# Kernel optimization log

Measured on AMD Instinct MI355X. Metric: run time of the kernel, lower is better.

Reference implementation:

```python
import jax, jax.numpy as jnp
import numpy as np

B, S, H, V = 2, 2048, 1024, 32000
SDS = [64, 128, 256]
EPS = 1e-5


def _ln(x, g, b):
    m = jnp.mean(x, -1, keepdims=True)
    v = jnp.var(x, -1, keepdims=True)
    return (x - m) * jax.lax.rsqrt(v + EPS) * g + b


def _layer(x, A_log, Wb, Wc, D, Wg, bg, Wo, bo, g, be):
    # x: [B,S,H]; state dim N = A_log.shape[0]
    A = jnp.exp(A_log)
    gate = jax.nn.sigmoid(jnp.einsum('bsh,nh->bsn', x, Wg) + bg)
    Bx = jnp.einsum('bsh,nh->bsn', x, Wb)
    u = gate * Bx  # [B,S,N]

    def step(s, u_t):
        s = A * s + u_t
        return s, s

    s0 = jnp.zeros((x.shape[0], A.shape[0]), x.dtype)
    _, states = jax.lax.scan(step, s0, jnp.swapaxes(u, 0, 1))  # [S,B,N]
    states = jnp.swapaxes(states, 0, 1)
    y = jnp.einsum('bsn,hn->bsh', states, Wc) + D * x
    out = _ln(y + x, g, be)
    return out @ Wo.T + bo  # dropout is identity (p used in eval / p=0)


def setup_inputs() -> dict:
    key = jax.random.key(0)
    ks = iter(jax.random.split(key, 64))
    d = {}
    d['x'] = jax.random.randint(next(ks), (B, S), 0, V)
    d['E'] = jax.random.normal(next(ks), (V, H), jnp.float32) * 0.02
    for i, N in enumerate(SDS):
        d[f'A{i}'] = jnp.log(jnp.exp(jnp.full((N,), -0.5)) + 0.1 * jax.random.normal(next(ks), (N,)))
        d[f'Wb{i}'] = jax.random.normal(next(ks), (N, H), jnp.float32) * 0.02
        d[f'Wc{i}'] = jax.random.normal(next(ks), (H, N), jnp.float32) * 0.02
        d[f'D{i}'] = jax.random.normal(next(ks), (H,), jnp.float32)
        d[f'Wg{i}'] = jax.random.normal(next(ks), (N, H), jnp.float32) * 0.02
        d[f'bg{i}'] = jnp.zeros((N,), jnp.float32)
        d[f'Wo{i}'] = jax.random.normal(next(ks), (H, H), jnp.float32) * 0.02
        d[f'bo{i}'] = jnp.zeros((H,), jnp.float32)
        d[f'g{i}'] = jnp.ones((H,), jnp.float32)
        d[f'be{i}'] = jnp.zeros((H,), jnp.float32)
    d['Wf'] = jax.random.normal(next(ks), (H, 3 * H), jnp.float32) * 0.02
    d['bf'] = jnp.zeros((H,), jnp.float32)
    d['gf'] = jnp.ones((H,), jnp.float32)
    d['bef'] = jnp.zeros((H,), jnp.float32)
    d['Wh'] = jax.random.normal(next(ks), (V, H), jnp.float32) * 0.02
    d['bh'] = jnp.zeros((V,), jnp.float32)
    return d


def reference(x, E,
              A0, Wb0, Wc0, D0, Wg0, bg0, Wo0, bo0, g0, be0,
              A1, Wb1, Wc1, D1, Wg1, bg1, Wo1, bo1, g1, be1,
              A2, Wb2, Wc2, D2, Wg2, bg2, Wo2, bo2, g2, be2,
              Wf, bf, gf, bef, Wh, bh):
    emb = E[x]  # [B,S,H]
    o0 = _layer(emb, A0, Wb0, Wc0, D0, Wg0, bg0, Wo0, bo0, g0, be0)
    o1 = _layer(emb, A1, Wb1, Wc1, D1, Wg1, bg1, Wo1, bo1, g1, be1)
    o2 = _layer(emb, A2, Wb2, Wc2, D2, Wg2, bg2, Wo2, bo2, g2, be2)
    combined = jnp.concatenate([o0, o1, o2], axis=-1)  # [B,S,3H]
    fused = combined @ Wf.T + bf
    fused = _ln(fused + emb, gf, bef)
    logits = fused @ Wh.T + bh  # [B,S,V]
    return logits
```

## Files before the change

### kernel.cpp

```cpp
#include <hip/hip_runtime.h>
#include <hip/hip_bf16.h>

#define Hd 1024
#define Bdim 2
#define Sd 2048
#define BSd 4096
#define Vd 32000
#define EPSf 1e-5f
#define CH 16
#define NCH 128
#define NT3 448

typedef __attribute__((ext_vector_type(8))) short short8;
typedef __attribute__((ext_vector_type(4))) float f32x4;
typedef __attribute__((ext_vector_type(4))) unsigned short us4;

__device__ __forceinline__ unsigned short f2bf(float f) {
  union { float f; unsigned int u; } v; v.f = f;
  return (unsigned short)((v.u + 0x7fffu + ((v.u >> 16) & 1u)) >> 16);
}

typedef __attribute__((address_space(1))) const void gvoid_t;
typedef __attribute__((address_space(3))) void svoid_t;
__device__ __forceinline__ void gl_lds16(const void* g, void* s) {
  __builtin_amdgcn_global_load_lds((gvoid_t*)g, (svoid_t*)s, 16, 0, 0);
}

struct CvtTab {
  const float* src[11];
  unsigned short* dst[11];
  int start[12];
};
__global__ void k_cvt_all(CvtTab tab) {
  int b = blockIdx.x;
  int j = 0;
  while (j < 10 && b >= tab.start[j + 1]) ++j;
  size_t i = (size_t)(b - tab.start[j]) * 256 + threadIdx.x;
  f32x4 v = *(const f32x4*)(tab.src[j] + i * 4);
  us4 o;
  o[0] = f2bf(v[0]); o[1] = f2bf(v[1]); o[2] = f2bf(v[2]); o[3] = f2bf(v[3]);
  *(us4*)(tab.dst[j] + i * 4) = o;
}

__global__ void k_cvtT(const float* __restrict__ s0, const float* __restrict__ s1,
                       const float* __restrict__ s2, unsigned short* __restrict__ dst) {
  const float* src = blockIdx.z == 0 ? s0 : (blockIdx.z == 1 ? s1 : s2);
  unsigned short* d = dst + (size_t)blockIdx.z * Hd * Hd;
  __shared__ float tile[32][33];
  int tx = threadIdx.x & 31, ty = threadIdx.x >> 5;
  int bx = blockIdx.x * 32, by = blockIdx.y * 32;
  #pragma unroll
  for (int i = 0; i < 4; ++i)
    tile[ty + i * 8][tx] = src[(size_t)(by + ty + i * 8) * Hd + bx + tx];
  __syncthreads();
  #pragma unroll
  for (int i = 0; i < 4; ++i)
    d[(size_t)(bx + ty + i * 8) * Hd + by + tx] = f2bf(tile[tx][ty + i * 8]);
}

__global__ void k_biasf(const float* __restrict__ Wf_, const float* __restrict__ bfb,
                        const float* __restrict__ bo0, const float* __restrict__ bo1,
                        const float* __restrict__ bo2, float* __restrict__ biasf) {
  int h = blockIdx.x, t = threadIdx.x;
  float s = 0.f;
  for (int c = t; c < 3072; c += 256) {
    float b = c < 1024 ? bo0[c] : (c < 2048 ? bo1[c - 1024] : bo2[c - 2048]);
    s += Wf_[(size_t)h * 3072 + c] * b;
  }
  #pragma unroll
  for (int o = 32; o >= 1; o >>= 1) s += __shfl_xor(s, o);
  __shared__ float red[4];
  if ((t & 63) == 0) red[t >> 6] = s;
  __syncthreads();
  if (t == 0) biasf[h] = bfb[h] + red[0] + red[1] + red[2] + red[3];
}

__global__ void k_setup(const float* A0, const float* A1, const float* A2,
                        const float* b0, const float* b1, const float* b2,
                        const float* D0, const float* D1, const float* D2,
                        const float* g0, const float* g1, const float* g2,
                        const float* e0, const float* e1, const float* e2,
                        float* Alog448, float* bg448,
                        float* D3, float* g3, float* be3) {
  int t = blockIdx.x * 256 + threadIdx.x;
  if (t < NT3) {
    int l = t < 64 ? 0 : (t < 192 ? 1 : 2);
    int o = t - (l == 0 ? 0 : (l == 1 ? 64 : 192));
    Alog448[t] = (l == 0 ? A0 : (l == 1 ? A1 : A2))[o];
    bg448[t]   = (l == 0 ? b0 : (l == 1 ? b1 : b2))[o];
  }
  if (t < 3072) {
    int l = t >> 10, o = t & 1023;
    D3[t]  = (l == 0 ? D0 : (l == 1 ? D1 : D2))[o];
    g3[t]  = (l == 0 ? g0 : (l == 1 ? g1 : g2))[o];
    be3[t] = (l == 0 ? e0 : (l == 1 ? e1 : e2))[o];
  }
}

__global__ void k_embed(const int* __restrict__ x, const float* __restrict__ E,
                        float* __restrict__ emb, unsigned short* __restrict__ embbf) {
  int row = blockIdx.x, t = threadIdx.x;
  int id = x[row];
  f32x4 v = *(const f32x4*)(E + (size_t)id * Hd + t * 4);
  *(f32x4*)(emb + (size_t)row * Hd + t * 4) = v;
  us4 o;
  o[0] = f2bf(v[0]); o[1] = f2bf(v[1]); o[2] = f2bf(v[2]); o[3] = f2bf(v[3]);
  *(us4*)(embbf + (size_t)row * Hd + t * 4) = o;
}

template<int BM, int BN, int WM, int WN, int BF16_OUT>
__launch_bounds__(WM * WN * 64)
__global__ void gemm2ph(const unsigned short* __restrict__ A,
                        const unsigned short* __restrict__ Bw,
                        const float* __restrict__ bias,
                        void* __restrict__ Cv,
                        int N, int K, int lda, int ldb, int ldc, int coff, int tm)
{
  constexpr int NT = WM * WN * 64;
  constexpr int MF = BM / WM / 16;
  constexpr int NF = BN / WN / 16;
  constexpr int ASZ = BM * 64;
  constexpr int BSZ = BN * 64;
  constexpr int AR = (ASZ * 2) / (NT * 16);
  constexpr int BR = (BSZ * 2) / (NT * 16);
  __shared__ __align__(16) unsigned short Sm[2 * (ASZ + BSZ)];

  int T = gridDim.x;
  int orig = blockIdx.x;
  int q = T >> 3, r = T & 7;
  int xc = orig & 7, sdv = orig >> 3;
  int wgid = (xc < r ? xc * (q + 1) : r * (q + 1) + (xc - r) * q) + sdv;
  int n_t = wgid / tm, m_t = wgid % tm;
  int row0 = m_t * BM, col0 = n_t * BN;

  int tid = threadIdx.x;
  int wave = tid >> 6, lane = tid & 63;
  int wm = wave / WN, wn = wave % WN;
  int wr = wm * (BM / WM), wc = wn * (BN / WN);
  int lr = lane & 15;
  int klane = lane >> 4;

  f32x4 acc[MF][NF] = {};

  auto stage = [&](int buf, int k0) {
    unsigned short* Ab = Sm + buf * (ASZ + BSZ);
    unsigned short* Bb = Ab + ASZ;
    #pragma unroll
    for (int j = 0; j < AR; ++j) {
      int slot = j * NT + tid;
      int lrow = slot >> 3, c16 = slot & 7;
      int scol = (c16 ^ (lrow & 7)) * 8;
      gl_lds16(A + (size_t)(row0 + lrow) * lda + k0 + scol, Ab + (j * NT + wave * 64) * 8);
    }
    #pragma unroll
    for (int j = 0; j < BR; ++j) {
      int slot = j * NT + tid;
      int lrow = slot >> 3, c16 = slot & 7;
      int scol = (c16 ^ (lrow & 7)) * 8;
      int brow = col0 + lrow;
      if (brow >= N) brow = N - 1;
      gl_lds16(Bw + (size_t)brow * ldb + k0 + scol, Bb + (j * NT + wave * 64) * 8);
    }
  };

  auto compute = [&](int buf) {
    const unsigned short* Ab = Sm + buf * (ASZ + BSZ);
    const unsigned short* Bb = Ab + ASZ;
    #pragma unroll
    for (int kk = 0; kk < 2; ++kk) {
      short8 afr[MF], bfr[NF];
      #pragma unroll
      for (int m = 0; m < MF; ++m) {
        int row = wr + m * 16 + lr;
        int cs = (kk * 4 + klane) ^ (row & 7);
        afr[m] = *(const short8*)(Ab + row * 64 + cs * 8);
      }
      #pragma unroll
      for (int n = 0; n < NF; ++n) {
        int row = wc + n * 16 + lr;
        int cs = (kk * 4 + klane) ^ (row & 7);
        bfr[n] = *(const short8*)(Bb + row * 64 + cs * 8);
      }
      #pragma unroll
      for (int m = 0; m < MF; ++m)
        #pragma unroll
        for (int n = 0; n < NF; ++n)
          acc[m][n] = __builtin_amdgcn_mfma_f32_16x16x32_bf16(afr[m], bfr[n], acc[m][n], 0, 0, 0);
    }
  };

  int nt = K >> 6;
  stage(0, 0);
  __syncthreads();
  for (int t = 0; t < nt - 1; ++t) {
    stage((t & 1) ^ 1, (t + 1) * 64);
    compute(t & 1);
    __syncthreads();
  }
  compute((nt - 1) & 1);

  int rb = (lane >> 4) * 4;
  #pragma unroll
  for (int m = 0; m < MF; ++m) {
    #pragma unroll
    for (int n = 0; n < NF; ++n) {
      int gcol = col0 + wc + n * 16 + lr;
      if (gcol >= N) continue;
      float bv = bias ? bias[gcol] : 0.f;
      #pragma unroll
      for (int j = 0; j < 4; ++j) {
        int grow = row0 + wr + m * 16 + rb + j;
        float val = acc[m][n][j] + bv;
        if (BF16_OUT)
          ((unsigned short*)Cv)[(size_t)grow * ldc + coff + gcol] = f2bf(val);
        else
          ((float*)Cv)[(size_t)grow * ldc + coff + gcol] = val;
      }
    }
  }
}

__launch_bounds__(512)
__global__ void gemm_ring(const unsigned short* __restrict__ A,
                          const unsigned short* __restrict__ Bw,
                          const float* __restrict__ bias,
                          float* __restrict__ Cv,
                          int N, int K, int lda, int ldb, int ldc, int tm)
{
  constexpr int ASZ = 256 * 32;
  constexpr int BUF = 2 * ASZ;
  __shared__ __align__(16) unsigned short Sm[4 * BUF];

  int T = gridDim.x;
  int orig = blockIdx.x;
  int q = T >> 3, r = T & 7;
  int xc = orig & 7, sdv = orig >> 3;
  int wgid = (xc < r ? xc * (q + 1) : r * (q + 1) + (xc - r) * q) + sdv;
  int n_t = wgid / tm, m_t = wgid % tm;
  int row0 = m_t * 256, col0 = n_t * 256;

  int tid = threadIdx.x;
  int wave = tid >> 6, lane = tid & 63;
  int wm = wave >> 2, wn = wave & 3;
  int wr = wm * 128, wc = wn * 64;
  int lr = lane & 15, klane = lane >> 4;

  f32x4 acc[8][4] = {};

  auto stage = [&](int buf, int kt) {
    int k0 = kt * 32;
    unsigned short* Ab = Sm + buf * BUF;
    unsigned short* Bb = Ab + ASZ;
    #pragma unroll
    for (int j = 0; j < 2; ++j) {
      int slot = j * 512 + wave * 64 + lane;
      int rrow = slot >> 2, ck = (slot & 3) * 8;
      gl_lds16(A + (size_t)(row0 + rrow) * lda + k0 + ck, Ab + (j * 512 + wave * 64) * 8);
    }
    #pragma unroll
    for (int j = 0; j < 2; ++j) {
      int slot = j * 512 + wave * 64 + lane;
      int rrow = slot >> 2, ck = (slot & 3) * 8;
      int brow = col0 + rrow;
      if (brow >= N) brow = N - 1;
      gl_lds16(Bw + (size_t)brow * ldb + k0 + ck, Bb + (j * 512 + wave * 64) * 8);
    }
  };

  auto compute = [&](int buf) {
    const unsigned short* Ab = Sm + buf * BUF;
    const unsigned short* Bb = Ab + ASZ;
    short8 afr[8], bfr[4];
    #pragma unroll
    for (int m = 0; m < 8; ++m)
      afr[m] = *(const short8*)(Ab + (wr + m * 16 + lr) * 32 + klane * 8);
    #pragma unroll
    for (int n = 0; n < 4; ++n)
      bfr[n] = *(const short8*)(Bb + (wc + n * 16 + lr) * 32 + klane * 8);
    __builtin_amdgcn_s_setprio(1);
    #pragma unroll
    for (int m = 0; m < 8; ++m)
      #pragma unroll
      for (int n = 0; n < 4; ++n)
        acc[m][n] = __builtin_amdgcn_mfma_f32_16x16x32_bf16(afr[m], bfr[n], acc[m][n], 0, 0, 0);
    __builtin_amdgcn_s_setprio(0);
  };

  int nt = K >> 5;
  stage(0, 0); stage(1, 1); stage(2, 2);
  for (int t = 0; t < nt; ++t) {
    if (t < nt - 2)       asm volatile("s_waitcnt vmcnt(8)" ::: "memory");
    else if (t == nt - 2) asm volatile("s_waitcnt vmcnt(4)" ::: "memory");
    else                  asm volatile("s_waitcnt vmcnt(0)" ::: "memory");
    __builtin_amdgcn_s_barrier();
    if (t + 3 < nt) stage((t + 3) & 3, t + 3);
    compute(t & 3);
  }

  int rb = (lane >> 4) * 4;
  #pragma unroll
  for (int m = 0; m < 8; ++m) {
    #pragma unroll
    for (int n = 0; n < 4; ++n) {
      int gcol = col0 + wc + n * 16 + lr;
      if (gcol >= N) continue;
      float bv = bias ? bias[gcol] : 0.f;
      #pragma unroll
      for (int j = 0; j < 4; ++j) {
        int grow = row0 + wr + m * 16 + rb + j;
        Cv[(size_t)grow * ldc + gcol] = acc[m][n][j] + bv;
      }
    }
  }
}

__global__ void k_scanA(const float* __restrict__ gzbx, const float* __restrict__ Alog448,
                        const float* __restrict__ bg448,
                        float* __restrict__ st, float* __restrict__ carry) {
  int gid = blockIdx.x * 256 + threadIdx.x;
  if (gid >= Bdim * NCH * NT3) return;
  int n = gid % NT3;
  int c = (gid / NT3) % NCH;
  int b = gid / (NT3 * NCH);
  float a = expf(Alog448[n]);
  float bgv = bg448[n];
  float s = 0.f;
  size_t rbase = (size_t)b * Sd + (size_t)c * CH;
  for (int t = 0; t < CH; ++t) {
    size_t row = rbase + t;
    float gzv = gzbx[row * 896 + n];
    float bxv = gzbx[row * 896 + 448 + n];
    float gv = 1.f / (1.f + expf(-(gzv + bgv)));
    s = a * s + gv * bxv;
    st[row * NT3 + n] = s;
  }
  carry[((size_t)b * NCH + c) * NT3 + n] = s;
}

__global__ void k_scanB(const float* __restrict__ carry, const float* __restrict__ Alog448,
                        float* __restrict__ cin) {
  int i = blockIdx.x * 256 + threadIdx.x;
  if (i >= Bdim * NT3) return;
  int b = i / NT3, n = i % NT3;
  float aC = expf((float)CH * Alog448[n]);
  float s = 0.f;
  for (int c = 0; c < NCH; ++c) {
    cin[((size_t)b * NCH + c) * NT3 + n] = s;
    s = aC * s + carry[((size_t)b * NCH + c) * NT3 + n];
  }
}

__global__ void k_scanC(const float* __restrict__ st, const float* __restrict__ cin,
                        const float* __restrict__ Alog448, unsigned short* __restrict__ stbf) {
  size_t gid = (size_t)blockIdx.x * 256 + threadIdx.x;
  if (gid >= (size_t)BSd * NT3) return;
  int n = gid % NT3;
  int row = gid / NT3;
  int b = row / Sd, sg = row % Sd;
  int c = sg / CH, t = sg % CH;
  float cv = cin[((size_t)b * NCH + c) * NT3 + n];
  float val = st[gid] + expf((float)(t + 1) * Alog448[n]) * cv;
  stbf[gid] = f2bf(val);
}

__global__ void k_ln3(const float* __restrict__ y3, const float* __restrict__ emb,
                      const float* __restrict__ D3, const float* __restrict__ g3,
                      const float* __restrict__ be3, unsigned short* __restrict__ z3) {
  int row = blockIdx.x, ly = blockIdx.y, t = threadIdx.x;
  const float* y = y3 + (size_t)row * 3072 + ly * 1024;
  f32x4 yv = *(const f32x4*)(y + t * 4);
  f32x4 ev = *(const f32x4*)(emb + (size_t)row * Hd + t * 4);
  float vals[4];
  float sum = 0.f, sq = 0.f;
  #pragma unroll
  for (int j = 0; j < 4; ++j) {
    float coef = D3[ly * 1024 + t * 4 + j] + 1.f;
    float v = yv[j] + coef * ev[j];
    vals[j] = v; sum += v; sq += v * v;
  }
  #pragma unroll
  for (int o = 32; o >= 1; o >>= 1) {
    sum += __shfl_xor(sum, o);
    sq += __shfl_xor(sq, o);
  }
  __shared__ float red[2][4];
  int w = t >> 6, lane = t & 63;
  if (lane == 0) { red[0][w] = sum; red[1][w] = sq; }
  __syncthreads();
  sum = red[0][0] + red[0][1] + red[0][2] + red[0][3];
  sq  = red[1][0] + red[1][1] + red[1][2] + red[1][3];
  float mean = sum * (1.f / Hd);
  float var = sq * (1.f / Hd) - mean * mean;
  float rs = rsqrtf(var + EPSf);
  us4 o4;
  #pragma unroll
  for (int j = 0; j < 4; ++j) {
    float z = (vals[j] - mean) * rs * g3[ly * 1024 + t * 4 + j] + be3[ly * 1024 + t * 4 + j];
    o4[j] = f2bf(z);
  }
  *(us4*)(z3 + (size_t)row * 3072 + ly * 1024 + t * 4) = o4;
}

__global__ void k_ln(const float* __restrict__ y, const float* __restrict__ emb,
                     const float* __restrict__ g, const float* __restrict__ be,
                     unsigned short* __restrict__ out) {
  int row = blockIdx.x, t = threadIdx.x;
  f32x4 yv = *(const f32x4*)(y + (size_t)row * Hd + t * 4);
  f32x4 ev = *(const f32x4*)(emb + (size_t)row * Hd + t * 4);
  float vals[4];
  float sum = 0.f, sq = 0.f;
  #pragma unroll
  for (int j = 0; j < 4; ++j) {
    float v = yv[j] + ev[j];
    vals[j] = v; sum += v; sq += v * v;
  }
  #pragma unroll
  for (int o = 32; o >= 1; o >>= 1) {
    sum += __shfl_xor(sum, o);
    sq += __shfl_xor(sq, o);
  }
  __shared__ float red[2][4];
  int w = t >> 6, lane = t & 63;
  if (lane == 0) { red[0][w] = sum; red[1][w] = sq; }
  __syncthreads();
  sum = red[0][0] + red[0][1] + red[0][2] + red[0][3];
  sq  = red[1][0] + red[1][1] + red[1][2] + red[1][3];
  float mean = sum * (1.f / Hd);
  float var = sq * (1.f / Hd) - mean * mean;
  float rs = rsqrtf(var + EPSf);
  us4 o4;
  #pragma unroll
  for (int j = 0; j < 4; ++j) {
    float z = (vals[j] - mean) * rs * g[t * 4 + j] + be[t * 4 + j];
    o4[j] = f2bf(z);
  }
  *(us4*)(out + (size_t)row * Hd + t * 4) = o4;
}

extern "C" void kernel_launch(void* const* d_in, const int* in_sizes, int n_in,
                              void* d_out, int out_size, void* d_ws, size_t ws_size,
                              hipStream_t stream) {
  (void)in_sizes; (void)n_in; (void)out_size; (void)ws_size;
  const int* x = (const int*)d_in[0];
  const float* E = (const float*)d_in[1];
  const float* Wf_ = (const float*)d_in[32];
  const float* bfb = (const float*)d_in[33];
  const float* gfp = (const float*)d_in[34];
  const float* bef = (const float*)d_in[35];
  const float* Wh_ = (const float*)d_in[36];
  const float* bh = (const float*)d_in[37];

  char* wsb = (char*)d_ws;
  size_t off = 0;
  auto alloc = [&](size_t bytes) -> void* {
    void* p = wsb + off;
    off += (bytes + 255) & ~(size_t)255;
    return p;
  };
  float* emb             = (float*)alloc((size_t)BSd * Hd * 4);
  unsigned short* embbf  = (unsigned short*)alloc((size_t)BSd * Hd * 2);
  unsigned short* wgwbbf = (unsigned short*)alloc((size_t)896 * Hd * 2);
  unsigned short* wcbf   = (unsigned short*)alloc((size_t)NT3 * Hd * 2);
  unsigned short* wotbf  = (unsigned short*)alloc((size_t)3 * Hd * Hd * 2);
  unsigned short* wfbf   = (unsigned short*)alloc((size_t)3 * Hd * Hd * 2);
  unsigned short* wcombbf= (unsigned short*)alloc((size_t)Hd * 3 * Hd * 2);
  unsigned short* whbf   = (unsigned short*)alloc((size_t)Vd * Hd * 2);
  float* gzbx            = (float*)alloc((size_t)BSd * 896 * 4);
  float* stl             = (float*)alloc((size_t)BSd * NT3 * 4);
  unsigned short* stbf   = (unsigned short*)alloc((size_t)BSd * NT3 * 2);
  float* carry           = (float*)alloc((size_t)Bdim * NCH * NT3 * 4);
  float* cin             = (float*)alloc((size_t)Bdim * NCH * NT3 * 4);
  float* ybuf3           = (float*)alloc((size_t)BSd * 3072 * 4);
  unsigned short* zbf3   = (unsigned short*)alloc((size_t)BSd * 3072 * 2);
  unsigned short* zbf    = (unsigned short*)alloc((size_t)BSd * Hd * 2);
  float* Alog448         = (float*)alloc(NT3 * 4);
  float* bg448           = (float*)alloc(NT3 * 4);
  float* D3              = (float*)alloc(3072 * 4);
  float* g3              = (float*)alloc(3072 * 4);
  float* be3             = (float*)alloc(3072 * 4);
  float* biasf           = (float*)alloc(Hd * 4);

  k_embed<<<BSd, 256, 0, stream>>>(x, E, emb, embbf);

  {
    CvtTab tab;
    const int rowoff_g[3] = {0, 64, 192};
    int j = 0;
    int n4s[11];
    for (int i = 0; i < 3; ++i) { tab.src[j] = (const float*)d_in[2 + 10 * i + 4]; tab.dst[j] = wgwbbf + (size_t)rowoff_g[i] * Hd;         n4s[j] = (64 << i) * Hd / 4; ++j; }
    for (int i = 0; i < 3; ++i) { tab.src[j] = (const float*)d_in[2 + 10 * i + 1]; tab.dst[j] = wgwbbf + (size_t)(448 + rowoff_g[i]) * Hd;  n4s[j] = (64 << i) * Hd / 4; ++j; }
    for (int i = 0; i < 3; ++i) { tab.src[j] = (const float*)d_in[2 + 10 * i + 2]; tab.dst[j] = wcbf + (size_t)rowoff_g[i] * Hd;            n4s[j] = (64 << i) * Hd / 4; ++j; }
    tab.src[j] = Wf_; tab.dst[j] = wfbf; n4s[j] = 3 * Hd * Hd / 4; ++j;
    tab.src[j] = Wh_; tab.dst[j] = whbf; n4s[j] = Vd * Hd / 4; ++j;
    tab.start[0] = 0;
    for (int k = 0; k < 11; ++k) tab.start[k + 1] = tab.start[k] + (n4s[k] + 255) / 256;
    k_cvt_all<<<tab.start[11], 256, 0, stream>>>(tab);
  }

  k_cvtT<<<dim3(32, 32, 3), 256, 0, stream>>>(
      (const float*)d_in[8], (const float*)d_in[18], (const float*)d_in[28], wotbf);

  k_setup<<<12, 256, 0, stream>>>(
      (const float*)d_in[2], (const float*)d_in[12], (const float*)d_in[22],
      (const float*)d_in[7], (const float*)d_in[17], (const float*)d_in[27],
      (const float*)d_in[5], (const float*)d_in[15], (const float*)d_in[25],
      (const float*)d_in[10], (const float*)d_in[20], (const float*)d_in[30],
      (const float*)d_in[11], (const float*)d_in[21], (const float*)d_in[31],
      Alog448, bg448, D3, g3, be3);

  k_biasf<<<Hd, 256, 0, stream>>>(Wf_, bfb,
      (const float*)d_in[9], (const float*)d_in[19], (const float*)d_in[29], biasf);

  for (int i = 0; i < 3; ++i) {
    gemm2ph<128,128,2,2,1><<<(Hd / 128) * (Hd / 128), 256, 0, stream>>>(
        wfbf + i * Hd, wotbf + (size_t)i * Hd * Hd, nullptr, wcombbf,
        Hd, Hd, 3 * Hd, Hd, 3 * Hd, i * Hd, Hd / 128);
  }

  const int TM = BSd / 128;

  gemm2ph<128,128,2,2,0><<<(896 / 128) * TM, 256, 0, stream>>>(
      embbf, wgwbbf, nullptr, gzbx, 896, Hd, Hd, Hd, 896, 0, TM);

  {
    int totA = Bdim * NCH * NT3;
    k_scanA<<<(totA + 255) / 256, 256, 0, stream>>>(gzbx, Alog448, bg448, stl, carry);
    k_scanB<<<(Bdim * NT3 + 255) / 256, 256, 0, stream>>>(carry, Alog448, cin);
    size_t totC = (size_t)BSd * NT3;
    k_scanC<<<(int)((totC + 255) / 256), 256, 0, stream>>>(stl, cin, Alog448, stbf);
  }

  const int owg[3] = {0, 64, 192};
  const int sd[3] = {64, 128, 256};
  for (int i = 0; i < 3; ++i) {
    gemm2ph<128,128,2,2,0><<<(Hd / 128) * TM, 256, 0, stream>>>(
        stbf + owg[i], wcbf + (size_t)owg[i] * Hd, nullptr, ybuf3,
        Hd, sd[i], NT3, sd[i], 3072, i * Hd, TM);
  }

  k_ln3<<<dim3(BSd, 3), 256, 0, stream>>>(ybuf3, emb, D3, g3, be3, zbf3);

  gemm2ph<128,128,2,2,0><<<(Hd / 128) * TM, 256, 0, stream>>>(
      zbf3, wcombbf, biasf, ybuf3, Hd, 3 * Hd, 3 * Hd, 3 * Hd, Hd, 0, TM);
  k_ln<<<BSd, 256, 0, stream>>>(ybuf3, emb, gfp, bef, zbf);

  const int TM256 = BSd / 256;
  gemm_ring<<<(Vd / 256) * TM256, 512, 0, stream>>>(
      zbf, whbf, bh, (float*)d_out, Vd, Hd, Hd, Hd, Vd, TM256);
}
```

Baseline: 648.7 us.

## Replace vocab-head GEMM with 8-phase ping-pong schedule and swizzled LDS

The final logits GEMM (4096x32000x1024) now uses K-tiles of 64 instead of 32, split into half-tiles, with an XOR-swizzled LDS layout meant to avoid bank conflicts. Each iteration runs eight barrier-separated phases that interleave LDS fragment reads, MFMA bursts and staged global-to-LDS loads across two buffers. The aim is finer overlap of memory traffic with MFMA work and fewer LDS conflicts on the dominant kernel. It drops the N-boundary clamping; 32000 divides by 256 so this holds here. It also adds many barriers and uses 128 KB of LDS.

```diff
diff --git a/kernel.cpp b/kernel.cpp
--- a/kernel.cpp
+++ b/kernel.cpp
@@ -221,15 +221,13 @@
 }
 
 __launch_bounds__(512)
-__global__ void gemm_ring(const unsigned short* __restrict__ A,
-                          const unsigned short* __restrict__ Bw,
-                          const float* __restrict__ bias,
-                          float* __restrict__ Cv,
-                          int N, int K, int lda, int ldb, int ldc, int tm)
+__global__ void gemm8ph(const unsigned short* __restrict__ A,
+                        const unsigned short* __restrict__ Bw,
+                        const float* __restrict__ bias,
+                        float* __restrict__ Cv,
+                        int N, int K, int lda, int ldb, int ldc, int tm)
 {
-  constexpr int ASZ = 256 * 32;
-  constexpr int BUF = 2 * ASZ;
-  __shared__ __align__(16) unsigned short Sm[4 * BUF];
+  __shared__ __align__(16) unsigned short Sm[65536];
 
   int T = gridDim.x;
   int orig = blockIdx.x;
@@ -242,76 +240,138 @@
   int tid = threadIdx.x;
   int wave = tid >> 6, lane = tid & 63;
   int wm = wave >> 2, wn = wave & 3;
-  int wr = wm * 128, wc = wn * 64;
   int lr = lane & 15, klane = lane >> 4;
 
   f32x4 acc[8][4] = {};
 
-  auto stage = [&](int buf, int kt) {
-    int k0 = kt * 32;
-    unsigned short* Ab = Sm + buf * BUF;
-    unsigned short* Bb = Ab + ASZ;
+  auto stageA = [&](int b, int h, int kt) {
+    unsigned short* base = Sm + (b * 2 + h) * 8192;
     #pragma unroll
     for (int j = 0; j < 2; ++j) {
-      int slot = j * 512 + wave * 64 + lane;
-      int rrow = slot >> 2, ck = (slot & 3) * 8;
-      gl_lds16(A + (size_t)(row0 + rrow) * lda + k0 + ck, Ab + (j * 512 + wave * 64) * 8);
-    }
+      int slot = j * 512 + tid;
+      int lrow = slot >> 3, c16 = slot & 7;
+      int scol = (c16 ^ (lrow & 7)) * 8;
+      gl_lds16(A + (size_t)(row0 + h * 128 + lrow) * lda + kt * 64 + scol,
+               base + (j * 512 + wave * 64) * 8);
+    }
+  };
+  auto stageB = [&](int b, int h, int kt) {
+    unsigned short* base = Sm + 32768 + (b * 2 + h) * 8192;
     #pragma unroll
     for (int j = 0; j < 2; ++j) {
-      int slot = j * 512 + wave * 64 + lane;
-      int rrow = slot >> 2, ck = (slot & 3) * 8;
-      int brow = col0 + rrow;
-      if (brow >= N) brow = N - 1;
-      gl_lds16(Bw + (size_t)brow * ldb + k0 + ck, Bb + (j * 512 + wave * 64) * 8);
+      int slot = j * 512 + tid;
+      int lrow = slot >> 3, c16 = slot & 7;
+      int scol = (c16 ^ (lrow & 7)) * 8;
+      gl_lds16(Bw + (size_t)(col0 + h * 128 + lrow) * ldb + kt * 64 + scol,
+               base + (j * 512 + wave * 64) * 8);
     }
   };
-
-  auto compute = [&](int buf) {
-    const unsigned short* Ab = Sm + buf * BUF;
-    const unsigned short* Bb = Ab + ASZ;
-    short8 afr[8], bfr[4];
-    #pragma unroll
-    for (int m = 0; m < 8; ++m)
-      afr[m] = *(const short8*)(Ab + (wr + m * 16 + lr) * 32 + klane * 8);
-    #pragma unroll
-    for (int n = 0; n < 4; ++n)
-      bfr[n] = *(const short8*)(Bb + (wc + n * 16 + lr) * 32 + klane * 8);
-    __builtin_amdgcn_s_setprio(1);
-    #pragma unroll
-    for (int m = 0; m < 8; ++m)
+  auto readA = [&](short8* afr, int b, int mh, int kk) {
+    const unsigned short* base = Sm + (b * 2 + mh) * 8192;
+    #pragma unroll
+    for (int f = 0; f < 4; ++f) {
+      int rowin = f * 32 + wm * 16 + lr;
+      int cs = (kk * 4 + klane) ^ (rowin & 7);
+      afr[f] = *(const short8*)(base + rowin * 64 + cs * 8);
+    }
+  };
+  auto readB = [&](short8* bfr, int b, int kk) {
+    #pragma unroll
+    for (int n = 0; n < 4; ++n) {
+      int rowin = (n & 1) * 64 + wn * 16 + lr;
+      const unsigned short* base = Sm + 32768 + (b * 2 + (n >> 1)) * 8192;
+      int cs = (kk * 4 + klane) ^ (rowin & 7);
+      bfr[n] = *(const short8*)(base + rowin * 64 + cs * 8);
+    }
+  };
+
+  #define MFMA16(mh, afr, bfr)                                                  \
+    __builtin_amdgcn_s_setprio(1);                                              \
+    _Pragma("unroll")                                                           \
+    for (int f = 0; f < 4; ++f)                                                 \
+      _Pragma("unroll")                                                         \
+      for (int n = 0; n < 4; ++n)                                               \
+        acc[(mh) * 4 + f][n] = __builtin_amdgcn_mfma_f32_16x16x32_bf16(         \
+            afr[f], bfr[n], acc[(mh) * 4 + f][n], 0, 0, 0);                     \
+    __builtin_amdgcn_s_setprio(0);
+
+  #define BAR()   __builtin_amdgcn_s_barrier()
+  #define FEN()   asm volatile("" ::: "memory")
+  #define VM4()   asm volatile("s_waitcnt vmcnt(4)" ::: "memory")
+  #define VM0()   asm volatile("s_waitcnt vmcnt(0)" ::: "memory")
+
+  int nt = K >> 6;
+  int iters = K >> 7;
+
+  stageA(0, 0, 0); stageB(0, 0, 0); stageB(0, 1, 0); stageA(0, 1, 0);
+  stageA(1, 0, 1); stageB(1, 0, 1);
+  VM4(); BAR();
+
+  short8 afr[4], bfr0[4], bfr1[4];
+  for (int i = 0; i < iters; ++i) {
+    int t1 = 2 * i + 1, t2 = 2 * i + 2, t3 = 2 * i + 3;
+    bool last = (i == iters - 1);
+    readA(afr, 0, 0, 0); readB(bfr0, 0, 0);
+    BAR(); FEN();
+    stageB(1, 1, t1); stageA(1, 1, t1);
+    MFMA16(0, afr, bfr0);
+    BAR();
+    readA(afr, 0, 0, 1); readB(bfr1, 0, 1);
+    BAR(); FEN();
+    MFMA16(0, afr, bfr1);
+    BAR();
+    readA(afr, 0, 1, 0);
+    BAR(); FEN();
+    if (t2 < nt) stageA(0, 0, t2);
+    MFMA16(1, afr, bfr0);
+    BAR();
+    readA(afr, 0, 1, 1);
+    BAR(); FEN();
+    if (t2 < nt) stageB(0, 0, t2);
+    MFMA16(1, afr, bfr1);
+    if (last) { VM0(); } else { VM4(); }
+    BAR();
+    readA(afr, 1, 0, 0); readB(bfr0, 1, 0);
+    BAR(); FEN();
+    if (t2 < nt) { stageB(0, 1, t2); stageA(0, 1, t2); }
+    MFMA16(0, afr, bfr0);
+    BAR();
+    readA(afr, 1, 0, 1); readB(bfr1, 1, 1);
+    BAR(); FEN();
+    MFMA16(0, afr, bfr1);
+    BAR();
+    readA(afr, 1, 1, 0);
+    BAR(); FEN();
+    if (t3 < nt) stageA(1, 0, t3);
+    MFMA16(1, afr, bfr0);
+    BAR();
+    readA(afr, 1, 1, 1);
+    BAR(); FEN();
+    if (t3 < nt) stageB(1, 0, t3);
+    MFMA16(1, afr, bfr1);
+    if (!last) { VM4(); }
+    BAR();
+  }
+
+  int rb = (lane >> 4) * 4;
+  #pragma unroll
+  for (int idx = 0; idx < 8; ++idx) {
+    int mh = idx >> 2, f = idx & 3;
+    int growb = row0 + mh * 128 + f * 32 + wm * 16 + rb;
+    #pragma unroll
+    for (int n = 0; n < 4; ++n) {
+      int gcol = col0 + (n & 1) * 64 + (n >> 1) * 128 + wn * 16 + lr;
+      float bv = bias[gcol];
       #pragma unroll
-      for (int n = 0; n < 4; ++n)
-        acc[m][n] = __builtin_amdgcn_mfma_f32_16x16x32_bf16(afr[m], bfr[n], acc[m][n], 0, 0, 0);
-    __builtin_amdgcn_s_setprio(0);
-  };
-
-  int nt = K >> 5;
-  stage(0, 0); stage(1, 1); stage(2, 2);
-  for (int t = 0; t < nt; ++t) {
-    if (t < nt - 2)       asm volatile("s_waitcnt vmcnt(8)" ::: "memory");
-    else if (t == nt - 2) asm volatile("s_waitcnt vmcnt(4)" ::: "memory");
-    else                  asm volatile("s_waitcnt vmcnt(0)" ::: "memory");
-    __builtin_amdgcn_s_barrier();
-    if (t + 3 < nt) stage((t + 3) & 3, t + 3);
-    compute(t & 3);
-  }
-
-  int rb = (lane >> 4) * 4;
-  #pragma unroll
-  for (int m = 0; m < 8; ++m) {
-    #pragma unroll
-    for (int n = 0; n < 4; ++n) {
-      int gcol = col0 + wc + n * 16 + lr;
-      if (gcol >= N) continue;
-      float bv = bias ? bias[gcol] : 0.f;
-      #pragma unroll
-      for (int j = 0; j < 4; ++j) {
-        int grow = row0 + wr + m * 16 + rb + j;
-        Cv[(size_t)grow * ldc + gcol] = acc[m][n][j] + bv;
-      }
-    }
-  }
+      for (int j = 0; j < 4; ++j)
+        Cv[(size_t)(growb + j) * ldc + gcol] = acc[idx][n][j] + bv;
+    }
+  }
+  #undef MFMA16
+  #undef BAR
+  #undef FEN
+  #undef VM4
+  #undef VM0
 }
 
 __global__ void k_scanA(const float* __restrict__ gzbx, const float* __restrict__ Alog448,
@@ -545,6 +605,6 @@
   k_ln<<<BSd, 256, 0, stream>>>(ybuf3, emb, gfp, bef, zbf);
 
   const int TM256 = BSd / 256;
-  gemm_ring<<<(Vd / 256) * TM256, 512, 0, stream>>>(
+  gemm8ph<<<(Vd / 256) * TM256, 512, 0, stream>>>(
       zbf, whbf, bh, (float*)d_out, Vd, Hd, Hd, Hd, Vd, TM256);
 }
```

New measurement: 620.3 us. 4.4% less time.
